# Performance work log

Hardware: AMD Instinct MI355X
Metric: run time of the kernel (lower is better)

## Reference

```python
import jax, jax.numpy as jnp
import numpy as np


def _gcn_conv(x, edge_index, W, b):
    """Faithful PyG GCNConv: add self-loops, symmetric norm, scatter-sum, bias."""
    n = x.shape[0]
    loop = jnp.arange(n, dtype=edge_index.dtype)
    src = jnp.concatenate([edge_index[0], loop])  # [E+n]
    dst = jnp.concatenate([edge_index[1], loop])
    # in-degree at dst (edge_weight = 1), as in gcn_norm
    deg = jax.ops.segment_sum(jnp.ones(src.shape[0], x.dtype), dst, num_segments=n)
    dinv = jnp.where(deg > 0, jax.lax.rsqrt(deg), 0.0)
    norm = dinv[src] * dinv[dst]                  # [E+n]
    h = x @ W                                     # [n, C] small GEMM
    msg = h[src] * norm[:, None]                  # gather + scale (dominant traffic)
    out = jax.ops.segment_sum(msg, dst, num_segments=n)  # scatter-sum
    return out + b


def setup_inputs() -> dict:
    key = jax.random.key(0)
    ks = jax.random.split(key, 8)
    N, E, C = 50000, 1000000, 64
    scale = 1.0 / np.sqrt(C)
    return {
        "x_star": jax.random.normal(ks[0], (N, C), jnp.float32),
        "x_gal": jax.random.normal(ks[1], (N, C), jnp.float32),
        "edge_ss_near": jax.random.randint(ks[2], (2, E), 0, N, jnp.int64),
        "edge_ss_far": jax.random.randint(ks[3], (2, E), 0, N, jnp.int64),
        "edge_gg_near": jax.random.randint(ks[4], (2, E), 0, N, jnp.int64),
        "W_ss_near": jax.random.normal(ks[5], (C, C), jnp.float32) * scale,
        "W_ss_far": jax.random.normal(ks[6], (C, C), jnp.float32) * scale,
        "W_gg_near": jax.random.normal(ks[7], (C, C), jnp.float32) * scale,
        "b_ss_near": jnp.zeros((C,), jnp.float32),
        "b_ss_far": jnp.zeros((C,), jnp.float32),
        "b_gg_near": jnp.zeros((C,), jnp.float32),
    }


def reference(x_star, x_gal, edge_ss_near, edge_ss_far, edge_gg_near,
              W_ss_near, W_ss_far, W_gg_near,
              b_ss_near, b_ss_far, b_gg_near):
    # HeteroConv with aggr='sum': per-edge-type GCNConv, summed per dst node type.
    out_star = (_gcn_conv(x_star, edge_ss_near, W_ss_near, b_ss_near)
                + _gcn_conv(x_star, edge_ss_far, W_ss_far, b_ss_far))
    out_gal = _gcn_conv(x_gal, edge_gg_near, W_gg_near, b_gg_near)
    return out_star, out_gal
```

## Files before the change

### kernel.cpp

```cpp
#include <hip/hip_runtime.h>
#include <hip/hip_fp16.h>

#define CCH 64
#define BKT 256
#define NBMAX 200
#define CAP 6144
#define PCH 8192
#define GR 64

typedef int int4a __attribute__((ext_vector_type(4), aligned(4)));

__device__ __forceinline__ int scan256ex(int v, int t, int* wsum) {
    int s = v;
    #pragma unroll
    for (int off = 1; off < 64; off <<= 1) {
        int u = __shfl_up(s, off, 64);
        if ((t & 63) >= off) s += u;
    }
    if ((t & 63) == 63) wsum[t >> 6] = s;
    __syncthreads();
    int wpre = 0;
    #pragma unroll
    for (int j = 0; j < 4; ++j) if (j < (t >> 6)) wpre += wsum[j];
    return wpre + s - v;
}

__global__ void __launch_bounds__(256) k_part(const int* __restrict__ e0,
        const int* __restrict__ e1, const int* __restrict__ e2,
        int* __restrict__ bucketcur, unsigned* __restrict__ bdata,
        int E, int NB) {
    int c = blockIdx.y;
    const int* ed = (c == 0) ? e0 : (c == 1) ? e1 : e2;
    int base = blockIdx.x * PCH;
    int nE = E - base; if (nE > PCH) nE = PCH;
    __shared__ unsigned stagedL[PCH];
    __shared__ int hist[NBMAX];
    __shared__ int cur[NBMAX];
    int t = threadIdx.x;
    if (t < NB) hist[t] = 0;
    __syncthreads();
    for (int k = t * 4; k < nE; k += 1024) {
        if (k + 3 < nE) {
            int4a s4 = *(const int4a*)(ed + base + k);
            int4a d4 = *(const int4a*)(ed + E + base + k);
            stagedL[k + 0] = (unsigned)s4.x | ((unsigned)d4.x << 16);
            stagedL[k + 1] = (unsigned)s4.y | ((unsigned)d4.y << 16);
            stagedL[k + 2] = (unsigned)s4.z | ((unsigned)d4.z << 16);
            stagedL[k + 3] = (unsigned)s4.w | ((unsigned)d4.w << 16);
            atomicAdd(&hist[d4.x >> 8], 1); atomicAdd(&hist[d4.y >> 8], 1);
            atomicAdd(&hist[d4.z >> 8], 1); atomicAdd(&hist[d4.w >> 8], 1);
        } else {
            for (int j = k; j < nE; ++j) {
                int s0 = ed[base + j];
                int d0 = ed[E + base + j];
                stagedL[j] = (unsigned)s0 | ((unsigned)d0 << 16);
                atomicAdd(&hist[d0 >> 8], 1);
            }
        }
    }
    __syncthreads();
    if (t < NB) {
        int v = hist[t];
        int old = atomicAdd(&bucketcur[c * NB + t], v);
        cur[t] = t * CAP + old;
    }
    __syncthreads();
    unsigned* bo = bdata + (size_t)c * NB * CAP;
    for (int k = t * 4; k < nE; k += 1024) {
        int kh = k + 4 < nE ? k + 4 : nE;
        int lim = (k + 4 < nE) ? k + 4 : nE;
        for (int j = k; j < lim; ++j) {
            unsigned rec = stagedL[j];
            int b = (int)(rec >> 24);
            int slot = atomicAdd(&cur[b], 1);
            bo[slot] = rec;
        }
        (void)kh;
    }
}

__global__ void __launch_bounds__(256) k_sort(const unsigned* __restrict__ bdata,
        const int* __restrict__ bucketcur, int* __restrict__ sdat,
        int* __restrict__ rst, int* __restrict__ ren, float* __restrict__ dinv,
        __half* __restrict__ zrow, int N, int NB) {
    int c = blockIdx.y, b = blockIdx.x;
    __shared__ unsigned staged[CAP];
    __shared__ unsigned sorted[CAP];
    __shared__ int cnt[BKT];
    __shared__ int cur[BKT];
    __shared__ int wsum[4];
    int t = threadIdx.x;
    if (c == 0 && b == 0 && t < 32) ((float*)zrow)[t] = 0.f;
    cnt[t] = 0;
    __syncthreads();
    int n = bucketcur[c * NB + b]; if (n > CAP) n = CAP;
    size_t g0 = (size_t)c * NB * CAP + (size_t)b * CAP;
    for (int i = t; i < n; i += 256) staged[i] = bdata[g0 + i];
    __syncthreads();
    for (int i = t; i < n; i += 256)
        atomicAdd(&cnt[(staged[i] >> 16) & 255], 1);
    __syncthreads();
    int v = cnt[t];
    int ex = scan256ex(v, t, wsum);
    cur[t] = ex;
    int row = b * BKT + t;
    if (row < N) {
        rst[c * N + row] = b * CAP + ex;
        ren[c * N + row] = b * CAP + ex + v;
        dinv[(size_t)c * N + row] = rsqrtf((float)(v + 1));
    }
    __syncthreads();
    for (int i = t; i < n; i += 256) {
        unsigned r = staged[i];
        int slot = atomicAdd(&cur[(r >> 16) & 255], 1);
        sorted[slot] = r & 0xFFFFu;
    }
    __syncthreads();
    int* so = sdat + (size_t)c * NB * CAP;
    for (int i = t; i < n; i += 256) so[g0 - (size_t)c * NB * CAP + i + 0] = (int)sorted[i];
}

__global__ void __launch_bounds__(256) k_gemm_all(const float* __restrict__ xs_,
        const float* __restrict__ xg_, const float* __restrict__ W0,
        const float* __restrict__ W1, const float* __restrict__ W2,
        const float* __restrict__ dinv, __half* __restrict__ h16, int N) {
    int star = (blockIdx.y == 0);
    const float* x = star ? xs_ : xg_;
    __shared__ float Ws[2][CCH * CCH];
    __shared__ float xT[CCH * (GR + 1)];
    int t = threadIdx.x;
    int row0 = blockIdx.x * GR;
    size_t NC = (size_t)N * CCH;
    if (star) {
        #pragma unroll
        for (int j = 0; j < 4; ++j) {
            int idx = j * 1024 + t * 4;
            *(float4*)(&Ws[0][idx]) = *(const float4*)(W0 + idx);
            *(float4*)(&Ws[1][idx]) = *(const float4*)(W1 + idx);
        }
    } else {
        #pragma unroll
        for (int j = 0; j < 4; ++j) {
            int idx = j * 1024 + t * 4;
            *(float4*)(&Ws[0][idx]) = *(const float4*)(W2 + idx);
        }
    }
    #pragma unroll
    for (int j = 0; j < 4; ++j) {
        int idx = t + j * 256;
        int r = idx >> 4;
        int c0 = (idx & 15) * 4;
        int row = row0 + r;
        float4 v = make_float4(0.f, 0.f, 0.f, 0.f);
        if (row < N) v = *(const float4*)(x + (size_t)row * CCH + c0);
        xT[(c0 + 0) * (GR + 1) + r] = v.x;
        xT[(c0 + 1) * (GR + 1) + r] = v.y;
        xT[(c0 + 2) * (GR + 1) + r] = v.z;
        xT[(c0 + 3) * (GR + 1) + r] = v.w;
    }
    __syncthreads();
    int c4 = (t & 15) * 4;
    int r0 = (t >> 4) * 4;
    if (star) {
        float4 a0 = make_float4(0.f, 0.f, 0.f, 0.f), a1 = a0, a2 = a0, a3 = a0;
        float4 d0 = a0, d1 = a0, d2 = a0, d3 = a0;
        #pragma unroll 4
        for (int k = 0; k < CCH; ++k) {
            float4 wv = *(float4*)(&Ws[0][k * CCH + c4]);
            float4 uv = *(float4*)(&Ws[1][k * CCH + c4]);
            float x0 = xT[k * (GR + 1) + r0 + 0];
            float x1 = xT[k * (GR + 1) + r0 + 1];
            float x2 = xT[k * (GR + 1) + r0 + 2];
            float x3 = xT[k * (GR + 1) + r0 + 3];
            a0.x += x0 * wv.x; a0.y += x0 * wv.y; a0.z += x0 * wv.z; a0.w += x0 * wv.w;
            a1.x += x1 * wv.x; a1.y += x1 * wv.y; a1.z += x1 * wv.z; a1.w += x1 * wv.w;
            a2.x += x2 * wv.x; a2.y += x2 * wv.y; a2.z += x2 * wv.z; a2.w += x2 * wv.w;
            a3.x += x3 * wv.x; a3.y += x3 * wv.y; a3.z += x3 * wv.z; a3.w += x3 * wv.w;
            d0.x += x0 * uv.x; d0.y += x0 * uv.y; d0.z += x0 * uv.z; d0.w += x0 * uv.w;
            d1.x += x1 * uv.x; d1.y += x1 * uv.y; d1.z += x1 * uv.z; d1.w += x1 * uv.w;
            d2.x += x2 * uv.x; d2.y += x2 * uv.y; d2.z += x2 * uv.z; d2.w += x2 * uv.w;
            d3.x += x3 * uv.x; d3.y += x3 * uv.y; d3.z += x3 * uv.z; d3.w += x3 * uv.w;
        }
        float4 av[4] = {a0, a1, a2, a3};
        float4 dv4[4] = {d0, d1, d2, d3};
        #pragma unroll
        for (int i = 0; i < 4; ++i) {
            int row = row0 + r0 + i;
            if (row < N) {
                float dd0 = dinv[row];
                float dd1 = dinv[N + row];
                union { __half2 h2[2]; float2 f2; } u;
                u.h2[0] = __floats2half2_rn(av[i].x * dd0, av[i].y * dd0);
                u.h2[1] = __floats2half2_rn(av[i].z * dd0, av[i].w * dd0);
                *(float2*)(h16 + (size_t)row * CCH + c4) = u.f2;
                u.h2[0] = __floats2half2_rn(dv4[i].x * dd1, dv4[i].y * dd1);
                u.h2[1] = __floats2half2_rn(dv4[i].z * dd1, dv4[i].w * dd1);
                *(float2*)(h16 + NC + (size_t)row * CCH + c4) = u.f2;
            }
        }
    } else {
        float4 a0 = make_float4(0.f, 0.f, 0.f, 0.f), a1 = a0, a2 = a0, a3 = a0;
        #pragma unroll 8
        for (int k = 0; k < CCH; ++k) {
            float4 wv = *(float4*)(&Ws[0][k * CCH + c4]);
            float x0 = xT[k * (GR + 1) + r0 + 0];
            float x1 = xT[k * (GR + 1) + r0 + 1];
            float x2 = xT[k * (GR + 1) + r0 + 2];
            float x3 = xT[k * (GR + 1) + r0 + 3];
            a0.x += x0 * wv.x; a0.y += x0 * wv.y; a0.z += x0 * wv.z; a0.w += x0 * wv.w;
            a1.x += x1 * wv.x; a1.y += x1 * wv.y; a1.z += x1 * wv.z; a1.w += x1 * wv.w;
            a2.x += x2 * wv.x; a2.y += x2 * wv.y; a2.z += x2 * wv.z; a2.w += x2 * wv.w;
            a3.x += x3 * wv.x; a3.y += x3 * wv.y; a3.z += x3 * wv.z; a3.w += x3 * wv.w;
        }
        float4 av[4] = {a0, a1, a2, a3};
        #pragma unroll
        for (int i = 0; i < 4; ++i) {
            int row = row0 + r0 + i;
            if (row < N) {
                float dd = dinv[2 * N + row];
                union { __half2 h2[2]; float2 f2; } u;
                u.h2[0] = __floats2half2_rn(av[i].x * dd, av[i].y * dd);
                u.h2[1] = __floats2half2_rn(av[i].z * dd, av[i].w * dd);
                *(float2*)(h16 + 2 * NC + (size_t)row * CCH + c4) = u.f2;
            }
        }
    }
}

__device__ __forceinline__ float4 gat4p(const __half* __restrict__ p, int l16) {
    union { float2 f2; __half2 h2[2]; } u;
    u.f2 = ((const float2*)p)[l16];
    float2 a = __half22float2(u.h2[0]);
    float2 b = __half22float2(u.h2[1]);
    return make_float4(a.x, a.y, b.x, b.y);
}

__device__ __forceinline__ void acc4(float4& a, float4 v) {
    a.x += v.x; a.y += v.y; a.z += v.z; a.w += v.w;
}

__global__ void __launch_bounds__(256) k_pull(const int* __restrict__ rst,
        const int* __restrict__ ren,
        const int* __restrict__ sdat, const __half* __restrict__ h16,
        const float* __restrict__ dinv, const __half* __restrict__ zrow,
        const float* __restrict__ b0, const float* __restrict__ b1,
        const float* __restrict__ b2,
        float* __restrict__ out, int N, int GAPE) {
    int row = blockIdx.x * 4 + (threadIdx.x >> 6);
    if (row >= 2 * N) return;
    int lane = threadIdx.x & 63;
    int q = lane >> 4;
    int l16 = lane & 15;
    size_t NC = (size_t)N * CCH;

    const __half* hcL;
    const int* sdL;
    int beg, end;
    float ddL;
    float4 bias;
    float* op;
    float4 acc = make_float4(0.f, 0.f, 0.f, 0.f);
    if (row < N) {
        int cv = q >> 1;
        int bg = rst[cv * N + row], eg = ren[cv * N + row];
        int mid = (bg + eg) >> 1;
        beg = (q & 1) ? mid : bg;
        end = (q & 1) ? eg : mid;
        hcL = h16 + (size_t)cv * NC;
        sdL = sdat + (size_t)cv * GAPE;
        ddL = dinv[cv * N + row];
        if (!(q & 1)) acc = gat4p(hcL + (size_t)row * CCH, l16);
        float4 bv0 = ((const float4*)b0)[l16];
        float4 bv1 = ((const float4*)b1)[l16];
        bias = make_float4(bv0.x + bv1.x, bv0.y + bv1.y,
                           bv0.z + bv1.z, bv0.w + bv1.w);
        op = out + (size_t)row * CCH;
    } else {
        int r = row - N;
        int bg = rst[2 * N + r], eg = ren[2 * N + r];
        int len = eg - bg;
        beg = bg + ((len * q) >> 2);
        end = bg + ((len * (q + 1)) >> 2);
        hcL = h16 + 2 * NC;
        sdL = sdat + 2 * (size_t)GAPE;
        ddL = dinv[2 * N + r];
        if (q == 0) acc = gat4p(hcL + (size_t)r * CCH, l16);
        bias = ((const float4*)b2)[l16];
        op = out + NC + (size_t)r * CCH;
    }

    int i = beg;
    for (; i + 7 < end; i += 8) {
        int4a q0 = *(const int4a*)(sdL + i);
        int4a q1 = *(const int4a*)(sdL + i + 4);
        float4 v0 = gat4p(hcL + (size_t)q0.x * CCH, l16);
        float4 v1 = gat4p(hcL + (size_t)q0.y * CCH, l16);
        float4 v2 = gat4p(hcL + (size_t)q0.z * CCH, l16);
        float4 v3 = gat4p(hcL + (size_t)q0.w * CCH, l16);
        float4 v4 = gat4p(hcL + (size_t)q1.x * CCH, l16);
        float4 v5 = gat4p(hcL + (size_t)q1.y * CCH, l16);
        float4 v6 = gat4p(hcL + (size_t)q1.z * CCH, l16);
        float4 v7 = gat4p(hcL + (size_t)q1.w * CCH, l16);
        acc4(acc, v0); acc4(acc, v1); acc4(acc, v2); acc4(acc, v3);
        acc4(acc, v4); acc4(acc, v5); acc4(acc, v6); acc4(acc, v7);
    }
    if (i < end) {
        int4a q0 = *(const int4a*)(sdL + i);
        int4a q1 = *(const int4a*)(sdL + i + 4);
        const __half* p0 = hcL + (size_t)q0.x * CCH;
        const __half* p1 = (i + 1 < end) ? hcL + (size_t)q0.y * CCH : zrow;
        const __half* p2 = (i + 2 < end) ? hcL + (size_t)q0.z * CCH : zrow;
        const __half* p3 = (i + 3 < end) ? hcL + (size_t)q0.w * CCH : zrow;
        const __half* p4 = (i + 4 < end) ? hcL + (size_t)q1.x * CCH : zrow;
        const __half* p5 = (i + 5 < end) ? hcL + (size_t)q1.y * CCH : zrow;
        const __half* p6 = (i + 6 < end) ? hcL + (size_t)q1.z * CCH : zrow;
        const __half* p7 = (i + 7 < end) ? hcL + (size_t)q1.w * CCH : zrow;
        float4 v0 = gat4p(p0, l16);
        float4 v1 = gat4p(p1, l16);
        float4 v2 = gat4p(p2, l16);
        float4 v3 = gat4p(p3, l16);
        float4 v4 = gat4p(p4, l16);
        float4 v5 = gat4p(p5, l16);
        float4 v6 = gat4p(p6, l16);
        float4 v7 = gat4p(p7, l16);
        acc4(acc, v0); acc4(acc, v1); acc4(acc, v2); acc4(acc, v3);
        acc4(acc, v4); acc4(acc, v5); acc4(acc, v6); acc4(acc, v7);
    }

    float4 t;
    t.x = acc.x * ddL; t.y = acc.y * ddL; t.z = acc.z * ddL; t.w = acc.w * ddL;
    t.x += __shfl_xor(t.x, 16, 64); t.y += __shfl_xor(t.y, 16, 64);
    t.z += __shfl_xor(t.z, 16, 64); t.w += __shfl_xor(t.w, 16, 64);
    t.x += __shfl_xor(t.x, 32, 64); t.y += __shfl_xor(t.y, 32, 64);
    t.z += __shfl_xor(t.z, 32, 64); t.w += __shfl_xor(t.w, 32, 64);
    if (lane < 16) {
        t.x += bias.x; t.y += bias.y; t.z += bias.z; t.w += bias.w;
        ((float4*)op)[l16] = t;
    }
}

static inline size_t align256(size_t x) { return (x + 255) & ~(size_t)255; }

extern "C" void kernel_launch(void* const* d_in, const int* in_sizes, int n_in,
                              void* d_out, int out_size, void* d_ws, size_t ws_size,
                              hipStream_t stream) {
    const float* x_star = (const float*)d_in[0];
    const float* x_gal  = (const float*)d_in[1];
    const int*   e_ssn  = (const int*)d_in[2];
    const int*   e_ssf  = (const int*)d_in[3];
    const int*   e_ggn  = (const int*)d_in[4];
    const float* W_ssn  = (const float*)d_in[5];
    const float* W_ssf  = (const float*)d_in[6];
    const float* W_ggn  = (const float*)d_in[7];
    const float* b_ssn  = (const float*)d_in[8];
    const float* b_ssf  = (const float*)d_in[9];
    const float* b_ggn  = (const float*)d_in[10];

    const int N  = in_sizes[0] / CCH;
    const int E  = in_sizes[2] / 2;
    const size_t NC = (size_t)N * CCH;
    const int NB   = (N + BKT - 1) / BKT;
    const int NBLK = (E + PCH - 1) / PCH;
    const int GAPE = NB * CAP;

    char* w = (char*)d_ws;
    __half*   h16    = (__half*)w;   w += align256((size_t)3 * NC * 2);
    float*    dinv   = (float*)w;    w += align256((size_t)3 * N * 4);
    unsigned* bdata  = (unsigned*)w; w += align256((size_t)3 * GAPE * 4);
    int*      sdat   = (int*)w;      w += align256((size_t)3 * GAPE * 4);
    int*      bucketcur = (int*)w;   w += align256((size_t)3 * NB * 4);
    int*      rst    = (int*)w;      w += align256((size_t)3 * N * 4);
    int*      ren    = (int*)w;      w += align256((size_t)3 * N * 4);
    __half*   zrow   = (__half*)w;   w += align256((size_t)CCH * 2);

    const int B = 256;

    hipMemsetAsync(bucketcur, 0, (size_t)3 * NB * 4, stream);
    k_part<<<dim3(NBLK, 3), B, 0, stream>>>(e_ssn, e_ssf, e_ggn,
                                            bucketcur, bdata, E, NB);
    k_sort<<<dim3(NB, 3), B, 0, stream>>>(bdata, bucketcur, sdat,
                                          rst, ren, dinv, zrow, N, NB);
    k_gemm_all<<<dim3((N + GR - 1) / GR, 2), B, 0, stream>>>(x_star, x_gal,
                                                             W_ssn, W_ssf, W_ggn,
                                                             dinv, h16, N);
    k_pull<<<(2 * N + 3) / 4, B, 0, stream>>>(rst, ren, sdat, h16, dinv, zrow,
                                              b_ssn, b_ssf, b_ggn,
                                              (float*)d_out, N, GAPE);
}
```

Before: 211.7 us.

## Fuse per-bucket sort with GEMM and split pull into two launches

Merges the bucket sort and the dense x@W transform into one kernel. Each sort block now also computes h for its 256 rows, reusing the in-degree counts in shared memory to form dinv instead of reading it back from global memory. Shared memory is overlaid between the sort buffers and the GEMM tiles. The star-side GEMM now recomputes the x tile once per edge type instead of sharing one x load across two weight matrices. The pull kernel is split into two launches over star and galaxy rows, which adds a launch and reduces sort-block occupancy because of the larger shared footprint.

```diff
diff --git a/kernel.cpp b/kernel.cpp
--- a/kernel.cpp
+++ b/kernel.cpp
@@ -67,7 +67,6 @@
     __syncthreads();
     unsigned* bo = bdata + (size_t)c * NB * CAP;
     for (int k = t * 4; k < nE; k += 1024) {
-        int kh = k + 4 < nE ? k + 4 : nE;
         int lim = (k + 4 < nE) ? k + 4 : nE;
         for (int j = k; j < lim; ++j) {
             unsigned rec = stagedL[j];
@@ -75,20 +74,27 @@
             int slot = atomicAdd(&cur[b], 1);
             bo[slot] = rec;
         }
-        (void)kh;
-    }
-}
-
-__global__ void __launch_bounds__(256) k_sort(const unsigned* __restrict__ bdata,
-        const int* __restrict__ bucketcur, int* __restrict__ sdat,
-        int* __restrict__ rst, int* __restrict__ ren, float* __restrict__ dinv,
-        __half* __restrict__ zrow, int N, int NB) {
+    }
+}
+
+#define SG_SMEM 51264
+__global__ void __launch_bounds__(256) k_sortgemm(
+        const unsigned* __restrict__ bdata, const int* __restrict__ bucketcur,
+        int* __restrict__ sdat, int* __restrict__ rst, int* __restrict__ ren,
+        float* __restrict__ dinv, __half* __restrict__ zrow,
+        const float* __restrict__ xs_, const float* __restrict__ xg_,
+        const float* __restrict__ W0, const float* __restrict__ W1,
+        const float* __restrict__ W2, __half* __restrict__ h16,
+        int N, int NB) {
     int c = blockIdx.y, b = blockIdx.x;
-    __shared__ unsigned staged[CAP];
-    __shared__ unsigned sorted[CAP];
-    __shared__ int cnt[BKT];
-    __shared__ int cur[BKT];
-    __shared__ int wsum[4];
+    __shared__ __align__(16) char smem[SG_SMEM];
+    int* cnt  = (int*)smem;
+    int* cur  = (int*)(smem + 1024);
+    int* wsum = (int*)(smem + 2048);
+    unsigned* staged = (unsigned*)(smem + 2112);
+    unsigned* sorted = (unsigned*)(smem + 26688);
+    float* Ws = (float*)(smem + 2112);
+    float* xT = (float*)(smem + 18496);
     int t = threadIdx.x;
     if (c == 0 && b == 0 && t < 32) ((float*)zrow)[t] = 0.f;
     cnt[t] = 0;
@@ -117,57 +123,41 @@
     }
     __syncthreads();
     int* so = sdat + (size_t)c * NB * CAP;
-    for (int i = t; i < n; i += 256) so[g0 - (size_t)c * NB * CAP + i + 0] = (int)sorted[i];
-}
-
-__global__ void __launch_bounds__(256) k_gemm_all(const float* __restrict__ xs_,
-        const float* __restrict__ xg_, const float* __restrict__ W0,
-        const float* __restrict__ W1, const float* __restrict__ W2,
-        const float* __restrict__ dinv, __half* __restrict__ h16, int N) {
-    int star = (blockIdx.y == 0);
-    const float* x = star ? xs_ : xg_;
-    __shared__ float Ws[2][CCH * CCH];
-    __shared__ float xT[CCH * (GR + 1)];
-    int t = threadIdx.x;
-    int row0 = blockIdx.x * GR;
+    for (int i = t; i < n; i += 256) so[(size_t)b * CAP + i] = (int)sorted[i];
+    __syncthreads();
+
+    const float* x = (c == 2) ? xg_ : xs_;
+    const float* W = (c == 0) ? W0 : (c == 1) ? W1 : W2;
     size_t NC = (size_t)N * CCH;
-    if (star) {
+    #pragma unroll
+    for (int j = 0; j < 4; ++j) {
+        int idx = j * 1024 + t * 4;
+        *(float4*)(Ws + idx) = *(const float4*)(W + idx);
+    }
+    __half* hc = h16 + (size_t)c * NC;
+    for (int ch = 0; ch < 4; ++ch) {
+        int row0 = b * BKT + ch * 64;
+        __syncthreads();
         #pragma unroll
         for (int j = 0; j < 4; ++j) {
-            int idx = j * 1024 + t * 4;
-            *(float4*)(&Ws[0][idx]) = *(const float4*)(W0 + idx);
-            *(float4*)(&Ws[1][idx]) = *(const float4*)(W1 + idx);
-        }
-    } else {
-        #pragma unroll
-        for (int j = 0; j < 4; ++j) {
-            int idx = j * 1024 + t * 4;
-            *(float4*)(&Ws[0][idx]) = *(const float4*)(W2 + idx);
-        }
-    }
-    #pragma unroll
-    for (int j = 0; j < 4; ++j) {
-        int idx = t + j * 256;
-        int r = idx >> 4;
-        int c0 = (idx & 15) * 4;
-        int row = row0 + r;
-        float4 v = make_float4(0.f, 0.f, 0.f, 0.f);
-        if (row < N) v = *(const float4*)(x + (size_t)row * CCH + c0);
-        xT[(c0 + 0) * (GR + 1) + r] = v.x;
-        xT[(c0 + 1) * (GR + 1) + r] = v.y;
-        xT[(c0 + 2) * (GR + 1) + r] = v.z;
-        xT[(c0 + 3) * (GR + 1) + r] = v.w;
-    }
-    __syncthreads();
-    int c4 = (t & 15) * 4;
-    int r0 = (t >> 4) * 4;
-    if (star) {
+            int idx = t + j * 256;
+            int r = idx >> 4;
+            int c0 = (idx & 15) * 4;
+            int rw = row0 + r;
+            float4 vv = make_float4(0.f, 0.f, 0.f, 0.f);
+            if (rw < N) vv = *(const float4*)(x + (size_t)rw * CCH + c0);
+            xT[(c0 + 0) * (GR + 1) + r] = vv.x;
+            xT[(c0 + 1) * (GR + 1) + r] = vv.y;
+            xT[(c0 + 2) * (GR + 1) + r] = vv.z;
+            xT[(c0 + 3) * (GR + 1) + r] = vv.w;
+        }
+        __syncthreads();
+        int c4 = (t & 15) * 4;
+        int r0 = (t >> 4) * 4;
         float4 a0 = make_float4(0.f, 0.f, 0.f, 0.f), a1 = a0, a2 = a0, a3 = a0;
-        float4 d0 = a0, d1 = a0, d2 = a0, d3 = a0;
-        #pragma unroll 4
+        #pragma unroll 8
         for (int k = 0; k < CCH; ++k) {
-            float4 wv = *(float4*)(&Ws[0][k * CCH + c4]);
-            float4 uv = *(float4*)(&Ws[1][k * CCH + c4]);
+            float4 wv = *(float4*)(Ws + k * CCH + c4);
             float x0 = xT[k * (GR + 1) + r0 + 0];
             float x1 = xT[k * (GR + 1) + r0 + 1];
             float x2 = xT[k * (GR + 1) + r0 + 2];
@@ -176,52 +166,17 @@
             a1.x += x1 * wv.x; a1.y += x1 * wv.y; a1.z += x1 * wv.z; a1.w += x1 * wv.w;
             a2.x += x2 * wv.x; a2.y += x2 * wv.y; a2.z += x2 * wv.z; a2.w += x2 * wv.w;
             a3.x += x3 * wv.x; a3.y += x3 * wv.y; a3.z += x3 * wv.z; a3.w += x3 * wv.w;
-            d0.x += x0 * uv.x; d0.y += x0 * uv.y; d0.z += x0 * uv.z; d0.w += x0 * uv.w;
-            d1.x += x1 * uv.x; d1.y += x1 * uv.y; d1.z += x1 * uv.z; d1.w += x1 * uv.w;
-            d2.x += x2 * uv.x; d2.y += x2 * uv.y; d2.z += x2 * uv.z; d2.w += x2 * uv.w;
-            d3.x += x3 * uv.x; d3.y += x3 * uv.y; d3.z += x3 * uv.z; d3.w += x3 * uv.w;
-        }
-        float4 av[4] = {a0, a1, a2, a3};
-        float4 dv4[4] = {d0, d1, d2, d3};
-        #pragma unroll
-        for (int i = 0; i < 4; ++i) {
-            int row = row0 + r0 + i;
-            if (row < N) {
-                float dd0 = dinv[row];
-                float dd1 = dinv[N + row];
-                union { __half2 h2[2]; float2 f2; } u;
-                u.h2[0] = __floats2half2_rn(av[i].x * dd0, av[i].y * dd0);
-                u.h2[1] = __floats2half2_rn(av[i].z * dd0, av[i].w * dd0);
-                *(float2*)(h16 + (size_t)row * CCH + c4) = u.f2;
-                u.h2[0] = __floats2half2_rn(dv4[i].x * dd1, dv4[i].y * dd1);
-                u.h2[1] = __floats2half2_rn(dv4[i].z * dd1, dv4[i].w * dd1);
-                *(float2*)(h16 + NC + (size_t)row * CCH + c4) = u.f2;
-            }
-        }
-    } else {
-        float4 a0 = make_float4(0.f, 0.f, 0.f, 0.f), a1 = a0, a2 = a0, a3 = a0;
-        #pragma unroll 8
-        for (int k = 0; k < CCH; ++k) {
-            float4 wv = *(float4*)(&Ws[0][k * CCH + c4]);
-            float x0 = xT[k * (GR + 1) + r0 + 0];
-            float x1 = xT[k * (GR + 1) + r0 + 1];
-            float x2 = xT[k * (GR + 1) + r0 + 2];
-            float x3 = xT[k * (GR + 1) + r0 + 3];
-            a0.x += x0 * wv.x; a0.y += x0 * wv.y; a0.z += x0 * wv.z; a0.w += x0 * wv.w;
-            a1.x += x1 * wv.x; a1.y += x1 * wv.y; a1.z += x1 * wv.z; a1.w += x1 * wv.w;
-            a2.x += x2 * wv.x; a2.y += x2 * wv.y; a2.z += x2 * wv.z; a2.w += x2 * wv.w;
-            a3.x += x3 * wv.x; a3.y += x3 * wv.y; a3.z += x3 * wv.z; a3.w += x3 * wv.w;
         }
         float4 av[4] = {a0, a1, a2, a3};
         #pragma unroll
         for (int i = 0; i < 4; ++i) {
-            int row = row0 + r0 + i;
-            if (row < N) {
-                float dd = dinv[2 * N + row];
+            int rw = row0 + r0 + i;
+            if (rw < N) {
+                float dd = rsqrtf((float)(cnt[ch * 64 + r0 + i] + 1));
                 union { __half2 h2[2]; float2 f2; } u;
                 u.h2[0] = __floats2half2_rn(av[i].x * dd, av[i].y * dd);
                 u.h2[1] = __floats2half2_rn(av[i].z * dd, av[i].w * dd);
-                *(float2*)(h16 + 2 * NC + (size_t)row * CCH + c4) = u.f2;
+                *(float2*)(hc + (size_t)rw * CCH + c4) = u.f2;
             }
         }
     }
@@ -245,8 +200,8 @@
         const float* __restrict__ dinv, const __half* __restrict__ zrow,
         const float* __restrict__ b0, const float* __restrict__ b1,
         const float* __restrict__ b2,
-        float* __restrict__ out, int N, int GAPE) {
-    int row = blockIdx.x * 4 + (threadIdx.x >> 6);
+        float* __restrict__ out, int N, int GAPE, int row0) {
+    int row = row0 + blockIdx.x * 4 + (threadIdx.x >> 6);
     if (row >= 2 * N) return;
     int lane = threadIdx.x & 63;
     int q = lane >> 4;
@@ -378,12 +333,14 @@
     hipMemsetAsync(bucketcur, 0, (size_t)3 * NB * 4, stream);
     k_part<<<dim3(NBLK, 3), B, 0, stream>>>(e_ssn, e_ssf, e_ggn,
                                             bucketcur, bdata, E, NB);
-    k_sort<<<dim3(NB, 3), B, 0, stream>>>(bdata, bucketcur, sdat,
-                                          rst, ren, dinv, zrow, N, NB);
-    k_gemm_all<<<dim3((N + GR - 1) / GR, 2), B, 0, stream>>>(x_star, x_gal,
-                                                             W_ssn, W_ssf, W_ggn,
-                                                             dinv, h16, N);
-    k_pull<<<(2 * N + 3) / 4, B, 0, stream>>>(rst, ren, sdat, h16, dinv, zrow,
-                                              b_ssn, b_ssf, b_ggn,
-                                              (float*)d_out, N, GAPE);
-}
+    k_sortgemm<<<dim3(NB, 3), B, 0, stream>>>(bdata, bucketcur, sdat,
+                                              rst, ren, dinv, zrow,
+                                              x_star, x_gal,
+                                              W_ssn, W_ssf, W_ggn, h16, N, NB);
+    k_pull<<<(N + 3) / 4, B, 0, stream>>>(rst, ren, sdat, h16, dinv, zrow,
+                                          b_ssn, b_ssf, b_ggn,
+                                          (float*)d_out, N, GAPE, 0);
+    k_pull<<<(N + 3) / 4, B, 0, stream>>>(rst, ren, sdat, h16, dinv, zrow,
+                                          b_ssn, b_ssf, b_ggn,
+                                          (float*)d_out, N, GAPE, N);
+}
```

New measurement: 221.5 us. +4.7%, slower.
